# Kernel tuning notes

Hardware: AMD Instinct MI355X
Metric: run time of the kernel (lower is better)

Reference implementation:

```python
import jax, jax.numpy as jnp
import numpy as np

ALPHA = 0.001  # plasticity learning rate from the source module
B, I, H = 64, 512, 1024
D = I + H


def _xavier(k, shape):
    fan_out, fan_in = shape
    lim = float(np.sqrt(6.0 / (fan_in + fan_out)))
    return jax.random.uniform(k, shape, minval=-lim, maxval=lim, dtype=jnp.float32)


def setup_inputs() -> dict:
    key = jax.random.key(0)
    ks = jax.random.split(key, 9)
    inputs = jax.random.normal(ks[0], (B, I), dtype=jnp.float32)
    hidden = 0.1 * jax.random.normal(ks[1], (B, H), dtype=jnp.float32)
    # per-sample plastic fast weights (nonzero to exercise the matvec path)
    wih = 0.01 * jax.random.normal(ks[2], (B, H, D), dtype=jnp.float32)
    Wih_a = _xavier(ks[3], (H, D))
    Wih_b = _xavier(ks[4], (H, D))
    Wih_c = _xavier(ks[5], (H, D))
    Wih_d = _xavier(ks[6], (H, D))
    bih = jnp.zeros((H,), dtype=jnp.float32)
    W_dop = _xavier(ks[7], (H, D))
    b_dop = jnp.zeros((H,), dtype=jnp.float32)
    return {"inputs": inputs, "hidden": hidden, "wih": wih,
            "Wih_a": Wih_a, "Wih_b": Wih_b, "Wih_c": Wih_c, "Wih_d": Wih_d,
            "bih": bih, "W_dop": W_dop, "b_dop": b_dop}


def reference(inputs, hidden, wih, Wih_a, Wih_b, Wih_c, Wih_d, bih, W_dop, b_dop):
    # x = cat(inputs, hidden): [B, D]
    x = jnp.concatenate([inputs, hidden], axis=1)
    # dopamine_signal is computed in the source but never used downstream;
    # kept here for fidelity (XLA will DCE it).
    _dopamine = jax.nn.sigmoid(x @ W_dop.T + b_dop)  # noqa: F841
    # batched matvec over the plastic fast weights: [B,H]
    new_hidden = jnp.tanh(jnp.einsum('bj,bkj->bk', x, wih) + bih)
    y = new_hidden[:, :, None]   # [B, H, 1]
    xb = x[:, None, :]           # [B, 1, D]
    # Hebbian outer-product update (the two 'ones' bmms are just broadcasts)
    wih_new = wih + ALPHA * (y * xb * Wih_a + xb * Wih_b + y * Wih_c + Wih_d)
    return new_hidden, wih_new
```

## Files before the change

kernel.cpp:

```cpp
#include <hip/hip_runtime.h>

constexpr int Bn = 64;
constexpr int In = 512;
constexpr int Hn = 1024;
constexpr int Dn = 1536;
constexpr float ALPHA = 0.001f;
constexpr int RPW = 16;

typedef float nfloat4 __attribute__((ext_vector_type(4)));

__global__ __launch_bounds__(256, 4) void prnn_fused_kernel(
    const float* __restrict__ inputs,
    const float* __restrict__ hidden,
    const float* __restrict__ wih,
    const float* __restrict__ Wa,
    const float* __restrict__ Wb,
    const float* __restrict__ Wc,
    const float* __restrict__ Wd,
    const float* __restrict__ bih,
    float* __restrict__ out_hidden,
    float* __restrict__ out_wih)
{
    __shared__ float4 sW[4 * (Dn / 4)];

    const int k   = blockIdx.x;
    const int tid = threadIdx.x;

    {
        const float4* wa4 = (const float4*)(Wa + (size_t)k * Dn);
        const float4* wb4 = (const float4*)(Wb + (size_t)k * Dn);
        const float4* wc4 = (const float4*)(Wc + (size_t)k * Dn);
        const float4* wd4 = (const float4*)(Wd + (size_t)k * Dn);
        #pragma unroll
        for (int e = 0; e < 2; ++e) {
            const int i = tid + e * 256;
            if (i < 384) {
                sW[i]        = wa4[i];
                sW[384 + i]  = wb4[i];
                sW[768 + i]  = wc4[i];
                sW[1152 + i] = wd4[i];
            }
        }
    }
    __syncthreads();

    const int wave = tid >> 6;
    const int lane = tid & 63;
    const int b0   = wave * RPW;
    const float bk = bih[k];
    const int base = lane * 4;

    float4 wbuf[3][6];
    float4 x[6];

    auto load_w = [&](int r, float4 (&w)[6]) {
        const float* __restrict__ wrow = wih + ((size_t)(b0 + r) * Hn + k) * Dn;
        #pragma unroll
        for (int c = 0; c < 6; ++c)
            w[c] = *(const float4*)(wrow + c * 256 + base);
    };

    load_w(0, wbuf[0]);
    load_w(1, wbuf[1]);

    #pragma unroll
    for (int r = 0; r < RPW; ++r) {
        const int b = b0 + r;

        {
            const float* __restrict__ xin  = inputs + b * In;
            const float* __restrict__ xhid = hidden + b * Hn;
            #pragma unroll
            for (int c = 0; c < 6; ++c) {
                const int idx = c * 256 + base;
                x[c] = (c < 2) ? *(const float4*)(xin + idx)
                               : *(const float4*)(xhid + (idx - In));
            }
        }
        if (r + 2 < RPW) load_w(r + 2, wbuf[(r + 2) % 3]);

        float4 (&w)[6] = wbuf[r % 3];

        float acc = 0.0f;
        #pragma unroll
        for (int c = 0; c < 6; ++c)
            acc += w[c].x * x[c].x + w[c].y * x[c].y
                 + w[c].z * x[c].z + w[c].w * x[c].w;

        #pragma unroll
        for (int off = 32; off > 0; off >>= 1)
            acc += __shfl_xor(acc, off, 64);

        const float y = tanhf(acc + bk);
        if (lane == 0) out_hidden[b * Hn + k] = y;

        float* __restrict__ orow = out_wih + ((size_t)b * Hn + k) * Dn;
        #pragma unroll
        for (int c = 0; c < 6; ++c) {
            const int e = c * 64 + lane;
            const float4 a4 = sW[e];
            const float4 b4 = sW[384 + e];
            const float4 c4 = sW[768 + e];
            const float4 d4 = sW[1152 + e];
            nfloat4 o;
            o.x = w[c].x + ALPHA * (y * x[c].x * a4.x + x[c].x * b4.x + y * c4.x + d4.x);
            o.y = w[c].y + ALPHA * (y * x[c].y * a4.y + x[c].y * b4.y + y * c4.y + d4.y);
            o.z = w[c].z + ALPHA * (y * x[c].z * a4.z + x[c].z * b4.z + y * c4.z + d4.z);
            o.w = w[c].w + ALPHA * (y * x[c].w * a4.w + x[c].w * b4.w + y * c4.w + d4.w);
            __builtin_nontemporal_store(o, (nfloat4*)(orow + c * 256 + base));
        }
    }
}

extern "C" void kernel_launch(void* const* d_in, const int* in_sizes, int n_in,
                              void* d_out, int out_size, void* d_ws, size_t ws_size,
                              hipStream_t stream) {
    const float* inputs = (const float*)d_in[0];
    const float* hidden = (const float*)d_in[1];
    const float* wih    = (const float*)d_in[2];
    const float* Wa     = (const float*)d_in[3];
    const float* Wb     = (const float*)d_in[4];
    const float* Wc     = (const float*)d_in[5];
    const float* Wd     = (const float*)d_in[6];
    const float* bih    = (const float*)d_in[7];

    float* out_hidden = (float*)d_out;
    float* out_wih    = (float*)d_out + (size_t)Bn * Hn;

    prnn_fused_kernel<<<dim3(Hn), dim3(256), 0, stream>>>(
        inputs, hidden, wih, Wa, Wb, Wc, Wd, bih, out_hidden, out_wih);
}
```

Baseline: 164.5 us.

## Batch four wih rows per load group and prescale plasticity weights by alpha

Restructures the per-wave loop so each wave loads four full wih rows (24 float4 loads) at once before computing, instead of a rolling three-deep prefetch. The intent is more memory-level parallelism per wave on this bandwidth-bound kernel. ALPHA is folded into the shared-memory copies of Wa..Wd and the update is refactored into two vector FMAs, which cuts ALU work per element. The occupancy hint of 4 blocks is dropped, so the larger register footprint may lower occupancy, and grouping loads removes overlap between groups, leaving a stall at the start of each group.

```diff
diff --git a/kernel.cpp b/kernel.cpp
--- a/kernel.cpp
+++ b/kernel.cpp
@@ -5,11 +5,10 @@
 constexpr int Hn = 1024;
 constexpr int Dn = 1536;
 constexpr float ALPHA = 0.001f;
-constexpr int RPW = 16;
 
 typedef float nfloat4 __attribute__((ext_vector_type(4)));
 
-__global__ __launch_bounds__(256, 4) void prnn_fused_kernel(
+__global__ __launch_bounds__(256) void prnn_fused_kernel(
     const float* __restrict__ inputs,
     const float* __restrict__ hidden,
     const float* __restrict__ wih,
@@ -21,24 +20,24 @@
     float* __restrict__ out_hidden,
     float* __restrict__ out_wih)
 {
-    __shared__ float4 sW[4 * (Dn / 4)];
+    __shared__ nfloat4 sW[4 * (Dn / 4)];
 
     const int k   = blockIdx.x;
     const int tid = threadIdx.x;
 
     {
-        const float4* wa4 = (const float4*)(Wa + (size_t)k * Dn);
-        const float4* wb4 = (const float4*)(Wb + (size_t)k * Dn);
-        const float4* wc4 = (const float4*)(Wc + (size_t)k * Dn);
-        const float4* wd4 = (const float4*)(Wd + (size_t)k * Dn);
+        const nfloat4* wa4 = (const nfloat4*)(Wa + (size_t)k * Dn);
+        const nfloat4* wb4 = (const nfloat4*)(Wb + (size_t)k * Dn);
+        const nfloat4* wc4 = (const nfloat4*)(Wc + (size_t)k * Dn);
+        const nfloat4* wd4 = (const nfloat4*)(Wd + (size_t)k * Dn);
         #pragma unroll
         for (int e = 0; e < 2; ++e) {
             const int i = tid + e * 256;
             if (i < 384) {
-                sW[i]        = wa4[i];
-                sW[384 + i]  = wb4[i];
-                sW[768 + i]  = wc4[i];
-                sW[1152 + i] = wd4[i];
+                sW[i]        = wa4[i] * ALPHA;
+                sW[384 + i]  = wb4[i] * ALPHA;
+                sW[768 + i]  = wc4[i] * ALPHA;
+                sW[1152 + i] = wd4[i] * ALPHA;
             }
         }
     }
@@ -46,68 +45,66 @@
 
     const int wave = tid >> 6;
     const int lane = tid & 63;
-    const int b0   = wave * RPW;
+    const int b0   = wave * 16;
     const float bk = bih[k];
     const int base = lane * 4;
 
-    float4 wbuf[3][6];
-    float4 x[6];
+    nfloat4 w[4][6];
+    nfloat4 xb[2][6];
 
-    auto load_w = [&](int r, float4 (&w)[6]) {
-        const float* __restrict__ wrow = wih + ((size_t)(b0 + r) * Hn + k) * Dn;
+    auto load_x = [&](int b, nfloat4 (&x)[6]) {
+        const float* __restrict__ xin  = inputs + b * In;
+        const float* __restrict__ xhid = hidden + b * Hn;
         #pragma unroll
-        for (int c = 0; c < 6; ++c)
-            w[c] = *(const float4*)(wrow + c * 256 + base);
+        for (int c = 0; c < 6; ++c) {
+            const int idx = c * 256 + base;
+            x[c] = (c < 2) ? *(const nfloat4*)(xin + idx)
+                           : *(const nfloat4*)(xhid + (idx - In));
+        }
     };
 
-    load_w(0, wbuf[0]);
-    load_w(1, wbuf[1]);
+    #pragma unroll
+    for (int g = 0; g < 4; ++g) {
+        const int bg = b0 + g * 4;
 
-    #pragma unroll
-    for (int r = 0; r < RPW; ++r) {
-        const int b = b0 + r;
+        #pragma unroll
+        for (int q = 0; q < 4; ++q) {
+            const float* __restrict__ wrow =
+                wih + ((size_t)(bg + q) * Hn + k) * Dn;
+            #pragma unroll
+            for (int c = 0; c < 6; ++c)
+                w[q][c] = *(const nfloat4*)(wrow + c * 256 + base);
+        }
+        load_x(bg, xb[0]);
 
-        {
-            const float* __restrict__ xin  = inputs + b * In;
-            const float* __restrict__ xhid = hidden + b * Hn;
+        #pragma unroll
+        for (int q = 0; q < 4; ++q) {
+            if (q < 3) load_x(bg + q + 1, xb[(q + 1) & 1]);
+            nfloat4 (&x)[6] = xb[q & 1];
+
+            float acc = 0.0f;
             #pragma unroll
             for (int c = 0; c < 6; ++c) {
-                const int idx = c * 256 + base;
-                x[c] = (c < 2) ? *(const float4*)(xin + idx)
-                               : *(const float4*)(xhid + (idx - In));
+                nfloat4 p = w[q][c] * x[c];
+                acc += (p.x + p.y) + (p.z + p.w);
             }
-        }
-        if (r + 2 < RPW) load_w(r + 2, wbuf[(r + 2) % 3]);
+            #pragma unroll
+            for (int off = 32; off > 0; off >>= 1)
+                acc += __shfl_xor(acc, off, 64);
 
-        float4 (&w)[6] = wbuf[r % 3];
+            const float y = tanhf(acc + bk);
+            const int b = bg + q;
+            if (lane == 0) out_hidden[b * Hn + k] = y;
 
-        float acc = 0.0f;
-        #pragma unroll
-        for (int c = 0; c < 6; ++c)
-            acc += w[c].x * x[c].x + w[c].y * x[c].y
-                 + w[c].z * x[c].z + w[c].w * x[c].w;
-
-        #pragma unroll
-        for (int off = 32; off > 0; off >>= 1)
-            acc += __shfl_xor(acc, off, 64);
-
-        const float y = tanhf(acc + bk);
-        if (lane == 0) out_hidden[b * Hn + k] = y;
-
-        float* __restrict__ orow = out_wih + ((size_t)b * Hn + k) * Dn;
-        #pragma unroll
-        for (int c = 0; c < 6; ++c) {
-            const int e = c * 64 + lane;
-            const float4 a4 = sW[e];
-            const float4 b4 = sW[384 + e];
-            const float4 c4 = sW[768 + e];
-            const float4 d4 = sW[1152 + e];
-            nfloat4 o;
-            o.x = w[c].x + ALPHA * (y * x[c].x * a4.x + x[c].x * b4.x + y * c4.x + d4.x);
-            o.y = w[c].y + ALPHA * (y * x[c].y * a4.y + x[c].y * b4.y + y * c4.y + d4.y);
-            o.z = w[c].z + ALPHA * (y * x[c].z * a4.z + x[c].z * b4.z + y * c4.z + d4.z);
-            o.w = w[c].w + ALPHA * (y * x[c].w * a4.w + x[c].w * b4.w + y * c4.w + d4.w);
-            __builtin_nontemporal_store(o, (nfloat4*)(orow + c * 256 + base));
+            float* __restrict__ orow = out_wih + ((size_t)b * Hn + k) * Dn;
+            #pragma unroll
+            for (int c = 0; c < 6; ++c) {
+                const int e = c * 64 + lane;
+                const nfloat4 m1 = x[c] * sW[e]       + sW[768 + e];
+                const nfloat4 m2 = x[c] * sW[384 + e] + sW[1152 + e];
+                const nfloat4 o  = (w[q][c] + m2) + y * m1;
+                __builtin_nontemporal_store(o, (nfloat4*)(orow + c * 256 + base));
+            }
         }
     }
 }
```

Measured after the change: 164.3 us. Within noise of the previous version (-0.1%).
